# Kernel optimization log

Measured on AMD Instinct MI355X. Metric: run time of the kernel, lower is better.

The kernel has to match this reference:

```python
import jax, jax.numpy as jnp
import numpy as np

BN_EPS = 1e-5


def setup_inputs() -> dict:
    key = jax.random.key(0)
    ks = jax.random.split(key, 6)
    P, D_IN, H, N_NODES = 2_000_000, 3, 128, 20_000
    x = jax.random.normal(ks[0], (P, D_IN), dtype=jnp.float32)
    batch_idx = jax.random.randint(ks[1], (P,), 0, N_NODES, dtype=jnp.int64)
    W1 = jax.random.normal(ks[2], (D_IN, H), dtype=jnp.float32) * 0.5
    b1 = jax.random.normal(ks[3], (H,), dtype=jnp.float32) * 0.1
    gamma = jnp.ones((H,), dtype=jnp.float32)
    beta = jnp.zeros((H,), dtype=jnp.float32)
    running_mean = jnp.zeros((H,), dtype=jnp.float32)
    running_var = jnp.ones((H,), dtype=jnp.float32)
    W2 = jax.random.normal(ks[4], (H, H), dtype=jnp.float32) * (1.0 / np.sqrt(H))
    b2 = jax.random.normal(ks[5], (H,), dtype=jnp.float32) * 0.1
    return {"x": x, "batch_idx": batch_idx, "num_nodes": N_NODES,
            "W1": W1, "b1": b1, "gamma": gamma, "beta": beta,
            "running_mean": running_mean, "running_var": running_var,
            "W2": W2, "b2": b2}


def reference(x, batch_idx, num_nodes, W1, b1, gamma, beta,
              running_mean, running_var, W2, b2):
    # per-point MLP: Linear -> BatchNorm1d (eval: running stats) -> ReLU -> Linear -> ReLU
    h = x @ W1 + b1                                        # [P, H]
    h = (h - running_mean) * jax.lax.rsqrt(running_var + BN_EPS) * gamma + beta
    h = jax.nn.relu(h)
    h = jax.nn.relu(h @ W2 + b2)                            # [P, H], values >= 0
    # scatter_max by node; torch_scatter fills empty segments with 0,
    # and since h >= 0 post-ReLU, clamping the -inf fill to 0 is exact.
    node_feats = jax.ops.segment_max(h, batch_idx, num_segments=num_nodes)
    return jnp.maximum(node_feats, 0.0)                     # [num_nodes, H]
```

## Files before the change

### kernel.cpp

```cpp
#include <hip/hip_runtime.h>
#include <hip/hip_bf16.h>

#define H 128
#define TILE_PTS 32
#define ROW_STRIDE 136
#define NBLK 512
#define BT 1024
#define BSH 4
#define NPB (1 << BSH)
#define CAP 2048
#define RAWN (CAP + 32)
#define HBUF (TILE_PTS * ROW_STRIDE)

typedef __attribute__((ext_vector_type(8))) short short8;
typedef __attribute__((ext_vector_type(4))) float float4v;
typedef __attribute__((ext_vector_type(2))) float float2v;
typedef __attribute__((ext_vector_type(4))) int int4v;
typedef _Float16 half8 __attribute__((ext_vector_type(8)));
typedef _Float16 half2 __attribute__((ext_vector_type(2)));

static __device__ __forceinline__ unsigned short f2bf(float f) {
    unsigned u = __float_as_uint(f);
    unsigned r = (u + 0x7fffu + ((u >> 16) & 1u)) >> 16;
    return (unsigned short)r;
}
static __device__ __forceinline__ unsigned pkbf(float a, float b) {
    __hip_bfloat162 h = __float22bfloat162_rn(float2{a, b});
    return *reinterpret_cast<unsigned*>(&h);
}
static __device__ __forceinline__ unsigned short f2h(float f) {
    _Float16 h = (_Float16)f;
    unsigned short u;
    __builtin_memcpy(&u, &h, 2);
    return u;
}
static __device__ __forceinline__ float h2f(unsigned short us) {
    _Float16 h;
    __builtin_memcpy(&h, &us, 2);
    return (float)h;
}

__global__ __launch_bounds__(BT)
void scatter_slot(const int* __restrict__ bidx, const float* __restrict__ x,
                  const float* __restrict__ W2, unsigned short* __restrict__ W2T,
                  int* __restrict__ gcnt, uint2* __restrict__ xb,
                  int P, int nbuk) {
    extern __shared__ int lh[];
    const int b = blockIdx.x, t = threadIdx.x;
    for (int i = b * BT + t; i < H * H; i += NBLK * BT) {
        int n = i >> 7, k = i & 127;
        W2T[i] = f2h(W2[k * H + n]);
    }
    for (int i = t; i < nbuk; i += BT) lh[i] = 0;
    __syncthreads();
    const int chunk4 = (((P + NBLK - 1) / NBLK) + 3) & ~3;
    const int lo = b * chunk4;
    const int hi = (lo + chunk4 < P) ? lo + chunk4 : P;
    for (int p4 = lo + 4 * t; p4 < hi; p4 += 4 * BT) {
        if (p4 + 4 <= hi) {
            int4v i4 = *(const int4v*)&bidx[p4];
            atomicAdd(&lh[i4.x >> BSH], 1);
            atomicAdd(&lh[i4.y >> BSH], 1);
            atomicAdd(&lh[i4.z >> BSH], 1);
            atomicAdd(&lh[i4.w >> BSH], 1);
        } else {
            for (int p = p4; p < hi; ++p) atomicAdd(&lh[bidx[p] >> BSH], 1);
        }
    }
    __syncthreads();
    for (int i = t; i < nbuk; i += BT) {
        int c = lh[i];
        lh[i] = (c > 0) ? atomicAdd(&gcnt[i], c) : 0;
    }
    __syncthreads();
    auto emit = [&](int idx, float x0, float x1, float x2) {
        int pos = atomicAdd(&lh[idx >> BSH], 1);
        if (pos < CAP) {
            uint2 r;
            r.x = (unsigned)f2h(x0) | ((unsigned)f2h(x1) << 16);
            r.y = (unsigned)f2h(x2) | ((unsigned)(idx & (NPB - 1)) << 16);
            xb[(size_t)(idx >> BSH) * CAP + pos] = r;
        }
    };
    for (int p4 = lo + 4 * t; p4 < hi; p4 += 4 * BT) {
        if (p4 + 4 <= hi) {
            int4v i4 = *(const int4v*)&bidx[p4];
            float4v xa = *(const float4v*)(x + (size_t)p4 * 3);
            float4v xbv = *(const float4v*)(x + (size_t)p4 * 3 + 4);
            float4v xc = *(const float4v*)(x + (size_t)p4 * 3 + 8);
            emit(i4.x, xa[0], xa[1], xa[2]);
            emit(i4.y, xa[3], xbv[0], xbv[1]);
            emit(i4.z, xbv[2], xbv[3], xc[0]);
            emit(i4.w, xc[1], xc[2], xc[3]);
        } else {
            for (int p = p4; p < hi; ++p)
                emit(bidx[p], x[p * 3 + 0], x[p * 3 + 1], x[p * 3 + 2]);
        }
    }
}

__global__ __launch_bounds__(256, 4)
void node_kernel13(const uint2* __restrict__ xb, const int* __restrict__ gcnt,
                   const float* __restrict__ W1, const float* __restrict__ b1,
                   const float* __restrict__ gamma, const float* __restrict__ beta,
                   const float* __restrict__ rmean, const float* __restrict__ rvar,
                   const unsigned short* __restrict__ W2T, const float* __restrict__ b2,
                   float* __restrict__ out, int N)
{
    __shared__ __align__(16) unsigned short pool[2 * HBUF];
    __shared__ __align__(16) uint2 srt[RAWN];
    __shared__ int basec[NPB + 1];
    __shared__ int cur[NPB];

    const int bk   = blockIdx.x;
    const int t    = threadIdx.x;
    const int lane = t & 63;
    const int wave = t >> 6;
    const int g  = t & 15;
    const int q  = t >> 4;
    const int c0 = g * 8;

    half2 w1h[3][4], b1h[4];
    #pragma unroll
    for (int jp = 0; jp < 4; ++jp) {
        #pragma unroll
        for (int e = 0; e < 2; ++e) {
            int c = c0 + 2 * jp + e;
            float sc = gamma[c] * rsqrtf(rvar[c] + 1e-5f);
            w1h[0][jp][e] = (_Float16)(W1[0 * H + c] * sc);
            w1h[1][jp][e] = (_Float16)(W1[1 * H + c] * sc);
            w1h[2][jp][e] = (_Float16)(W1[2 * H + c] * sc);
            b1h[jp][e]    = (_Float16)((b1[c] - rmean[c]) * sc + beta[c]);
        }
    }

    const int bn = lane & 15;
    const int kq = (lane >> 4) * 8;
    half8 bfrag[2][4];
    float  b2v[2];
    #pragma unroll
    for (int nt = 0; nt < 2; ++nt) {
        const int nn = wave * 32 + nt * 16 + bn;
        b2v[nt] = b2[nn];
        #pragma unroll
        for (int kk = 0; kk < 4; ++kk)
            bfrag[nt][kk] = *(const half8*)(const void*)&W2T[nn * H + kk * 32 + kq];
    }

    uint2* raw = (uint2*)pool;
    int n_b = gcnt[bk];
    if (n_b > CAP) n_b = CAP;
    const uint2* src = xb + (size_t)bk * CAP;
    for (int p = t; p < n_b; p += 256) raw[p] = src[p];
    if (t < NPB) cur[t] = 0;
    __syncthreads();
    for (int p = t; p < n_b; p += 256)
        atomicAdd(&cur[raw[p].y >> 16], 1);
    __syncthreads();
    if (t == 0) {
        int run = 0;
        #pragma unroll
        for (int i = 0; i < NPB; ++i) { int c = cur[i]; basec[i] = run; run += c; }
        basec[NPB] = run;
    }
    __syncthreads();
    if (t < NPB) cur[t] = basec[t];
    __syncthreads();
    for (int p = t; p < n_b; p += 256) {
        uint2 r = raw[p];
        int pos = atomicAdd(&cur[r.y >> 16], 1);
        srt[pos] = r;
    }
    for (int p = n_b + t; p < n_b + TILE_PTS; p += 256)
        if (p < RAWN) srt[p] = uint2{0u, 0u};
    __syncthreads();

    const float4v zero4 = {0.f, 0.f, 0.f, 0.f};
    const float NEG_INF = -__builtin_inff();
    const half2 zero2h = {(_Float16)0.f, (_Float16)0.f};
    const int nodebase = bk << BSH;
    const int nlocal = (N - nodebase < NPB) ? (N - nodebase) : NPB;

    const int st0 = q * ROW_STRIDE + c0;
    const int st1 = (q + 16) * ROW_STRIDE + c0;
    const int ar  = bn * ROW_STRIDE + kq;

    #define STAGE_PT(r, hs, so)                                            \
    {                                                                      \
        half2 a0 = __builtin_bit_cast(half2,                               \
            __builtin_amdgcn_perm(0u, (r).x, 0x01000100u));                \
        half2 a1 = __builtin_bit_cast(half2,                               \
            __builtin_amdgcn_perm(0u, (r).x, 0x03020302u));                \
        half2 a2 = __builtin_bit_cast(half2,                               \
            __builtin_amdgcn_perm(0u, (r).y, 0x01000100u));                \
        int4v pk;                                                          \
        _Pragma("unroll")                                                  \
        for (int jp = 0; jp < 4; ++jp) {                                   \
            half2 hh = b1h[jp];                                            \
            hh = __builtin_elementwise_fma(a0, w1h[0][jp], hh);            \
            hh = __builtin_elementwise_fma(a1, w1h[1][jp], hh);            \
            hh = __builtin_elementwise_fma(a2, w1h[2][jp], hh);            \
            hh = __builtin_elementwise_max(hh, zero2h);                    \
            pk[jp] = __builtin_bit_cast(int, hh);                          \
        }                                                                  \
        *(int4v*)(void*)&(hs)[so] = pk;                                    \
    }

    for (int j = 0; j < nlocal; ++j) {
        const int startj = basec[j];
        const int n      = basec[j + 1] - startj;
        const int ntiles = (n + TILE_PTS - 1) >> 5;

        float2v vm0 = {NEG_INF, NEG_INF};
        float2v vm1 = {NEG_INF, NEG_INF};

        if (ntiles > 0) {
            unsigned short* hb = pool;
            unsigned short* hs = pool + HBUF;
            {
                uint2 r0 = srt[startj + q];
                uint2 r1 = srt[startj + q + 16];
                STAGE_PT(r0, hb, st0);
                STAGE_PT(r1, hb, st1);
            }
            __syncthreads();

            for (int tile = 0; tile < ntiles; ++tile) {
                const int tb = tile * TILE_PTS;
                const bool have = (tile + 1 < ntiles);

                uint2 n0, n1;
                if (have) {
                    n0 = srt[startj + tb + TILE_PTS + q];
                    n1 = srt[startj + tb + TILE_PTS + 16 + q];
                }

                float4v acc00, acc01, acc10, acc11;
                {
                    half8 a0v = *(const half8*)(const void*)&hb[ar];
                    half8 a1v = *(const half8*)(const void*)&hb[ar + 16 * ROW_STRIDE];
                    acc00 = __builtin_amdgcn_mfma_f32_16x16x32_f16(a0v, bfrag[0][0], zero4, 0, 0, 0);
                    acc01 = __builtin_amdgcn_mfma_f32_16x16x32_f16(a0v, bfrag[1][0], zero4, 0, 0, 0);
                    acc10 = __builtin_amdgcn_mfma_f32_16x16x32_f16(a1v, bfrag[0][0], zero4, 0, 0, 0);
                    acc11 = __builtin_amdgcn_mfma_f32_16x16x32_f16(a1v, bfrag[1][0], zero4, 0, 0, 0);
                }
                #pragma unroll
                for (int kk = 1; kk < 4; ++kk) {
                    half8 a0v = *(const half8*)(const void*)&hb[ar + kk * 32];
                    half8 a1v = *(const half8*)(const void*)&hb[ar + 16 * ROW_STRIDE + kk * 32];
                    acc00 = __builtin_amdgcn_mfma_f32_16x16x32_f16(a0v, bfrag[0][kk], acc00, 0, 0, 0);
                    acc01 = __builtin_amdgcn_mfma_f32_16x16x32_f16(a0v, bfrag[1][kk], acc01, 0, 0, 0);
                    acc10 = __builtin_amdgcn_mfma_f32_16x16x32_f16(a1v, bfrag[0][kk], acc10, 0, 0, 0);
                    acc11 = __builtin_amdgcn_mfma_f32_16x16x32_f16(a1v, bfrag[1][kk], acc11, 0, 0, 0);
                }

                if (have) {
                    STAGE_PT(n0, hs, st0);
                    STAGE_PT(n1, hs, st1);
                }

                if (tb + TILE_PTS <= n) {
                    vm0 = __builtin_elementwise_max(vm0, float2v{acc00[0], acc00[1]});
                    vm0 = __builtin_elementwise_max(vm0, float2v{acc00[2], acc00[3]});
                    vm0 = __builtin_elementwise_max(vm0, float2v{acc10[0], acc10[1]});
                    vm0 = __builtin_elementwise_max(vm0, float2v{acc10[2], acc10[3]});
                    vm1 = __builtin_elementwise_max(vm1, float2v{acc01[0], acc01[1]});
                    vm1 = __builtin_elementwise_max(vm1, float2v{acc01[2], acc01[3]});
                    vm1 = __builtin_elementwise_max(vm1, float2v{acc11[0], acc11[1]});
                    vm1 = __builtin_elementwise_max(vm1, float2v{acc11[2], acc11[3]});
                } else {
                    const int r0base = (lane >> 4) * 4;
                    #pragma unroll
                    for (int r = 0; r < 4; ++r) {
                        const bool v0 = (tb + r0base + r) < n;
                        const bool v1 = (tb + 16 + r0base + r) < n;
                        vm0[r & 1] = fmaxf(vm0[r & 1], v0 ? acc00[r] : NEG_INF);
                        vm1[r & 1] = fmaxf(vm1[r & 1], v0 ? acc01[r] : NEG_INF);
                        vm0[r & 1] = fmaxf(vm0[r & 1], v1 ? acc10[r] : NEG_INF);
                        vm1[r & 1] = fmaxf(vm1[r & 1], v1 ? acc11[r] : NEG_INF);
                    }
                }
                __syncthreads();
                unsigned short* tmp = hb; hb = hs; hs = tmp;
            }
        }

        float vmax0 = fmaxf(vm0[0], vm0[1]);
        float vmax1 = fmaxf(vm1[0], vm1[1]);
        vmax0 = fmaxf(vmax0, __shfl_xor(vmax0, 16, 64));
        vmax0 = fmaxf(vmax0, __shfl_xor(vmax0, 32, 64));
        vmax1 = fmaxf(vmax1, __shfl_xor(vmax1, 16, 64));
        vmax1 = fmaxf(vmax1, __shfl_xor(vmax1, 32, 64));
        if (lane < 16) {
            float* orow = out + (size_t)(nodebase + j) * H + wave * 32;
            orow[lane]      = fmaxf(vmax0 + b2v[0], 0.f);
            orow[16 + lane] = fmaxf(vmax1 + b2v[1], 0.f);
        }
    }
    #undef STAGE_PT
}

__global__ void histB_kernel(const int* __restrict__ bidx, int* __restrict__ counts, int P) {
    int p = blockIdx.x * 256 + threadIdx.x;
    if (p < P) atomicAdd(&counts[bidx[p]], 1);
}
__global__ __launch_bounds__(1024)
void scanB_kernel(const int* __restrict__ counts, int* __restrict__ starts,
                  int* __restrict__ cursor, int N) {
    __shared__ int sums[1024];
    const int t = threadIdx.x;
    const int chunk = (N + 1023) >> 10;
    const int lo = t * chunk;
    const int hi = (lo + chunk < N) ? lo + chunk : N;
    int s = 0;
    for (int i = lo; i < hi; ++i) s += counts[i];
    sums[t] = s;
    __syncthreads();
    #pragma unroll
    for (int off = 1; off < 1024; off <<= 1) {
        int a = (t >= off) ? sums[t - off] : 0;
        __syncthreads();
        sums[t] += a;
        __syncthreads();
    }
    int run = sums[t] - s;
    for (int i = lo; i < hi; ++i) { starts[i] = run; cursor[i] = run; run += counts[i]; }
    if (t == 1023) starts[N] = sums[1023];
}
__global__ void scatterB_kernel(const int* __restrict__ bidx, const float* __restrict__ x,
                                int* __restrict__ cursor, uint2* __restrict__ xs, int P) {
    int p = blockIdx.x * 256 + threadIdx.x;
    if (p < P) {
        int pos = atomicAdd(&cursor[bidx[p]], 1);
        uint2 r;
        r.x = (unsigned)f2h(x[p * 3 + 0]) | ((unsigned)f2h(x[p * 3 + 1]) << 16);
        r.y = (unsigned)f2h(x[p * 3 + 2]);
        xs[pos] = r;
    }
}
__global__ void convw2_kernel(const float* __restrict__ W2, unsigned short* __restrict__ W2T) {
    int i = blockIdx.x * 256 + threadIdx.x;
    if (i < H * H) {
        int n = i >> 7, k = i & 127;
        W2T[i] = f2bf(W2[k * H + n]);
    }
}

__global__ __launch_bounds__(256, 4)
void node_kernelB(const uint2* __restrict__ xs,
                  const int*   __restrict__ starts,
                  const float* __restrict__ W1, const float* __restrict__ b1,
                  const float* __restrict__ gamma, const float* __restrict__ beta,
                  const float* __restrict__ rmean, const float* __restrict__ rvar,
                  const unsigned short* __restrict__ W2T, const float* __restrict__ b2,
                  float* __restrict__ out, int N)
{
    __shared__ __align__(16) unsigned short h1s[2][TILE_PTS * ROW_STRIDE];
    const int t = threadIdx.x, lane = t & 63, wave = t >> 6;
    const int g = t & 15, q = t >> 4, c0 = g * 8;
    float2v w1f2[3][4], b1f2[4];
    #pragma unroll
    for (int jp = 0; jp < 4; ++jp)
        #pragma unroll
        for (int e = 0; e < 2; ++e) {
            int c = c0 + 2 * jp + e;
            float sc = gamma[c] * rsqrtf(rvar[c] + 1e-5f);
            w1f2[0][jp][e] = W1[0 * H + c] * sc;
            w1f2[1][jp][e] = W1[1 * H + c] * sc;
            w1f2[2][jp][e] = W1[2 * H + c] * sc;
            b1f2[jp][e]    = (b1[c] - rmean[c]) * sc + beta[c];
        }
    const int bn = lane & 15, kq = (lane >> 4) * 8;
    short8 bfrag[2][4]; float b2v[2];
    #pragma unroll
    for (int nt = 0; nt < 2; ++nt) {
        const int nn = wave * 32 + nt * 16 + bn;
        b2v[nt] = b2[nn];
        #pragma unroll
        for (int kk = 0; kk < 4; ++kk)
            bfrag[nt][kk] = *(const short8*)&W2T[nn * H + kk * 32 + kq];
    }
    const float4v zero4 = {0.f, 0.f, 0.f, 0.f};
    const float NEG_INF = -__builtin_inff();
    const float2v zero2 = {0.f, 0.f};
    for (int node = blockIdx.x; node < N; node += gridDim.x) {
        const int start = starts[node];
        const int n = starts[node + 1] - start;
        const int ntiles = (n + TILE_PTS - 1) >> 5;
        float2v vmax2[2];
        vmax2[0] = float2v{NEG_INF, NEG_INF};
        vmax2[1] = float2v{NEG_INF, NEG_INF};
        auto loadx = [&](int tb, float xv[2][3]) {
            #pragma unroll
            for (int i = 0; i < 2; ++i) {
                uint2 r = xs[start + tb + q + 16 * i];
                xv[i][0] = h2f((unsigned short)(r.x & 0xffffu));
                xv[i][1] = h2f((unsigned short)(r.x >> 16));
                xv[i][2] = h2f((unsigned short)(r.y & 0xffffu));
            }
        };
        auto stage = [&](const float xv[2][3], unsigned short* buf) {
            #pragma unroll
            for (int i = 0; i < 2; ++i) {
                const int pl = q + 16 * i;
                float2v a0 = {xv[i][0], xv[i][0]};
                float2v a1 = {xv[i][1], xv[i][1]};
                float2v a2 = {xv[i][2], xv[i][2]};
                int4v pk;
                #pragma unroll
                for (int jp = 0; jp < 4; ++jp) {
                    float2v h = b1f2[jp];
                    h = __builtin_elementwise_fma(a0, w1f2[0][jp], h);
                    h = __builtin_elementwise_fma(a1, w1f2[1][jp], h);
                    h = __builtin_elementwise_fma(a2, w1f2[2][jp], h);
                    h = __builtin_elementwise_max(h, zero2);
                    pk[jp] = (int)pkbf(h[0], h[1]);
                }
                *(int4v*)(void*)&buf[pl * ROW_STRIDE + c0] = pk;
            }
        };
        if (ntiles > 0) {
            float xv[2][3];
            loadx(0, xv);
            stage(xv, h1s[0]);
            __syncthreads();
            int pb = 0;
            for (int tile = 0; tile < ntiles; ++tile) {
                const int tb = tile * TILE_PTS;
                const bool havenext = (tile + 1 < ntiles);
                float nx[2][3];
                if (havenext) loadx(tb + TILE_PTS, nx);
                float4v acc[2][2];
                const unsigned short* hb = h1s[pb];
                {
                    short8 a0 = *(const short8*)&hb[bn * ROW_STRIDE + kq];
                    short8 a1 = *(const short8*)&hb[(16 + bn) * ROW_STRIDE + kq];
                    #pragma unroll
                    for (int nt = 0; nt < 2; ++nt) {
                        acc[0][nt] = __builtin_amdgcn_mfma_f32_16x16x32_bf16(a0, bfrag[nt][0], zero4, 0, 0, 0);
                        acc[1][nt] = __builtin_amdgcn_mfma_f32_16x16x32_bf16(a1, bfrag[nt][0], zero4, 0, 0, 0);
                    }
                }
                #pragma unroll
                for (int kk = 1; kk < 4; ++kk) {
                    short8 a0 = *(const short8*)&hb[bn * ROW_STRIDE + kk * 32 + kq];
                    short8 a1 = *(const short8*)&hb[(16 + bn) * ROW_STRIDE + kk * 32 + kq];
                    #pragma unroll
                    for (int nt = 0; nt < 2; ++nt) {
                        acc[0][nt] = __builtin_amdgcn_mfma_f32_16x16x32_bf16(a0, bfrag[nt][kk], acc[0][nt], 0, 0, 0);
                        acc[1][nt] = __builtin_amdgcn_mfma_f32_16x16x32_bf16(a1, bfrag[nt][kk], acc[1][nt], 0, 0, 0);
                    }
                }
                if (havenext) stage(nx, h1s[pb ^ 1]);
                if (tb + TILE_PTS <= n) {
                    #pragma unroll
                    for (int ps = 0; ps < 2; ++ps)
                        #pragma unroll
                        for (int nt = 0; nt < 2; ++nt) {
                            vmax2[nt] = __builtin_elementwise_max(vmax2[nt],
                                          float2v{acc[ps][nt][0], acc[ps][nt][1]});
                            vmax2[nt] = __builtin_elementwise_max(vmax2[nt],
                                          float2v{acc[ps][nt][2], acc[ps][nt][3]});
                        }
                } else {
                    #pragma unroll
                    for (int ps = 0; ps < 2; ++ps)
                        #pragma unroll
                        for (int r = 0; r < 4; ++r) {
                            const int pl = ps * 16 + (lane >> 4) * 4 + r;
                            const bool valid = (tb + pl) < n;
                            vmax2[0][r & 1] = fmaxf(vmax2[0][r & 1], valid ? acc[ps][0][r] : NEG_INF);
                            vmax2[1][r & 1] = fmaxf(vmax2[1][r & 1], valid ? acc[ps][1][r] : NEG_INF);
                        }
                }
                __syncthreads();
                pb ^= 1;
            }
        }
        float vmax0 = fmaxf(vmax2[0][0], vmax2[0][1]);
        float vmax1 = fmaxf(vmax2[1][0], vmax2[1][1]);
        vmax0 = fmaxf(vmax0, __shfl_xor(vmax0, 16, 64));
        vmax0 = fmaxf(vmax0, __shfl_xor(vmax0, 32, 64));
        vmax1 = fmaxf(vmax1, __shfl_xor(vmax1, 16, 64));
        vmax1 = fmaxf(vmax1, __shfl_xor(vmax1, 32, 64));
        if (lane < 16) {
            float* orow = out + (size_t)node * H + wave * 32;
            orow[lane]      = fmaxf(vmax0 + b2v[0], 0.f);
            orow[16 + lane] = fmaxf(vmax1 + b2v[1], 0.f);
        }
    }
}

extern "C" void kernel_launch(void* const* d_in, const int* in_sizes, int n_in,
                              void* d_out, int out_size, void* d_ws, size_t ws_size,
                              hipStream_t stream) {
    const float* x     = (const float*)d_in[0];
    const int*   bidx  = (const int*)  d_in[1];
    const float* W1    = (const float*)d_in[3];
    const float* b1    = (const float*)d_in[4];
    const float* gamma = (const float*)d_in[5];
    const float* beta  = (const float*)d_in[6];
    const float* rmean = (const float*)d_in[7];
    const float* rvar  = (const float*)d_in[8];
    const float* W2    = (const float*)d_in[9];
    const float* b2    = (const float*)d_in[10];
    float* out = (float*)d_out;

    const int P = in_sizes[1];
    const int N = out_size / H;
    const int nbuk = (N + NPB - 1) >> BSH;

    const size_t szW2T = 32768;
    const size_t szG   = (size_t)4 * ((nbuk + 63) & ~63);
    const size_t szXb  = (size_t)8 * ((size_t)CAP * nbuk + 64);
    const size_t needA = szW2T + szG + szXb + 256;
    const size_t lds1  = (size_t)4 * nbuk;

    char* w = (char*)d_ws;

    if (lds1 <= 60000 && ws_size >= needA) {
        unsigned short* W2T = (unsigned short*)w;
        int* gcnt = (int*)(w + szW2T);
        uint2* xb = (uint2*)(w + szW2T + szG);

        hipMemsetAsync(gcnt, 0, (size_t)nbuk * sizeof(int), stream);
        scatter_slot<<<NBLK, BT, lds1, stream>>>(bidx, x, W2, W2T, gcnt, xb, P, nbuk);
        node_kernel13<<<nbuk, 256, 0, stream>>>(xb, gcnt, W1, b1, gamma, beta,
                                                rmean, rvar, W2T, b2, out, N);
        return;
    }

    const int Npad = (N + 63) & ~63;
    const size_t szStarts = (size_t)4 * (Npad + 64);
    const size_t szCnt    = (size_t)4 * Npad;
    const size_t szRec    = (size_t)8 * (P + 64);
    const size_t needB    = szStarts + szW2T + 2 * szCnt + szRec + 256;
    if (ws_size >= needB) {
        int* starts = (int*)w;
        unsigned short* W2T = (unsigned short*)(w + szStarts);
        int* counts = (int*)(w + szStarts + szW2T);
        int* cursor = (int*)(w + szStarts + szW2T + szCnt);
        uint2* xs   = (uint2*)(w + szStarts + szW2T + 2 * szCnt);

        hipMemsetAsync(counts, 0, (size_t)N * sizeof(int), stream);
        const int pblocks = (P + 255) / 256;
        const int grid = (N < 2048) ? N : 2048;
        convw2_kernel<<<(H * H + 255) / 256, 256, 0, stream>>>(W2, W2T);
        histB_kernel<<<pblocks, 256, 0, stream>>>(bidx, counts, P);
        scanB_kernel<<<1, 1024, 0, stream>>>(counts, starts, cursor, N);
        scatterB_kernel<<<pblocks, 256, 0, stream>>>(bidx, x, cursor, xs, P);
        node_kernelB<<<grid, 256, 0, stream>>>(xs, starts, W1, b1, gamma, beta,
                                               rmean, rvar, W2T, b2, out, N);
    }
}
```

Measured before the change: 217.0 us.

## Switch second-layer GEMM to 32x32x16 MFMA with XOR-swizzled LDS staging

Replaces the four 16x16x32 f16 MFMA accumulators per wave with a single 32x32x16 f16 MFMA chain over eight K-steps. Each lane now owns one output column, so the segment-max reduction needs one shuffle instead of four. The staged hidden rows in LDS are XOR-swizzled to avoid bank conflicts under the new A-fragment read pattern. This trades MFMA shape and register layout for fewer LDS reads and cheaper reductions, at the risk of a longer-latency dependent MFMA chain.

Measured after the change: 223.9 us. 3.1% more time.

```diff
diff --git a/kernel.cpp b/kernel.cpp
--- a/kernel.cpp
+++ b/kernel.cpp
@@ -16,6 +16,7 @@
 typedef __attribute__((ext_vector_type(4))) float float4v;
 typedef __attribute__((ext_vector_type(2))) float float2v;
 typedef __attribute__((ext_vector_type(4))) int int4v;
+typedef __attribute__((ext_vector_type(16))) float f32x16;
 typedef _Float16 half8 __attribute__((ext_vector_type(8)));
 typedef _Float16 half2 __attribute__((ext_vector_type(2)));
 
@@ -100,7 +101,7 @@
 }
 
 __global__ __launch_bounds__(256, 4)
-void node_kernel13(const uint2* __restrict__ xb, const int* __restrict__ gcnt,
+void node_kernel15(const uint2* __restrict__ xb, const int* __restrict__ gcnt,
                    const float* __restrict__ W1, const float* __restrict__ b1,
                    const float* __restrict__ gamma, const float* __restrict__ beta,
                    const float* __restrict__ rmean, const float* __restrict__ rvar,
@@ -134,18 +135,14 @@
         }
     }
 
-    const int bn = lane & 15;
-    const int kq = (lane >> 4) * 8;
-    half8 bfrag[2][4];
-    float  b2v[2];
+    const int col   = lane & 31;
+    const int khalf = lane >> 5;
+    const int nn = wave * 32 + col;
+    half8 bfrag[8];
+    float b2v = b2[nn];
     #pragma unroll
-    for (int nt = 0; nt < 2; ++nt) {
-        const int nn = wave * 32 + nt * 16 + bn;
-        b2v[nt] = b2[nn];
-        #pragma unroll
-        for (int kk = 0; kk < 4; ++kk)
-            bfrag[nt][kk] = *(const half8*)(const void*)&W2T[nn * H + kk * 32 + kq];
-    }
+    for (int kk = 0; kk < 8; ++kk)
+        bfrag[kk] = *(const half8*)(const void*)&W2T[nn * H + kk * 16 + khalf * 8];
 
     uint2* raw = (uint2*)pool;
     int n_b = gcnt[bk];
@@ -175,15 +172,17 @@
         if (p < RAWN) srt[p] = uint2{0u, 0u};
     __syncthreads();
 
-    const float4v zero4 = {0.f, 0.f, 0.f, 0.f};
+    const f32x16 zero16 = {0.f,0.f,0.f,0.f,0.f,0.f,0.f,0.f,
+                           0.f,0.f,0.f,0.f,0.f,0.f,0.f,0.f};
     const float NEG_INF = -__builtin_inff();
     const half2 zero2h = {(_Float16)0.f, (_Float16)0.f};
     const int nodebase = bk << BSH;
     const int nlocal = (N - nodebase < NPB) ? (N - nodebase) : NPB;
 
-    const int st0 = q * ROW_STRIDE + c0;
-    const int st1 = (q + 16) * ROW_STRIDE + c0;
-    const int ar  = bn * ROW_STRIDE + kq;
+    const int swz_st = ((q >> 3) & 1) << 3;
+    const int st0 = q * ROW_STRIDE + (c0 ^ swz_st);
+    const int st1 = (q + 16) * ROW_STRIDE + (c0 ^ swz_st);
+    const int arS = col * ROW_STRIDE + ((khalf ^ ((col >> 3) & 1)) * 8);
 
     #define STAGE_PT(r, hs, so)                                            \
     {                                                                      \
@@ -211,8 +210,7 @@
         const int n      = basec[j + 1] - startj;
         const int ntiles = (n + TILE_PTS - 1) >> 5;
 
-        float2v vm0 = {NEG_INF, NEG_INF};
-        float2v vm1 = {NEG_INF, NEG_INF};
+        float vmx = NEG_INF;
 
         if (ntiles > 0) {
             unsigned short* hb = pool;
@@ -235,23 +233,15 @@
                     n1 = srt[startj + tb + TILE_PTS + 16 + q];
                 }
 
-                float4v acc00, acc01, acc10, acc11;
+                f32x16 acc;
                 {
-                    half8 a0v = *(const half8*)(const void*)&hb[ar];
-                    half8 a1v = *(const half8*)(const void*)&hb[ar + 16 * ROW_STRIDE];
-                    acc00 = __builtin_amdgcn_mfma_f32_16x16x32_f16(a0v, bfrag[0][0], zero4, 0, 0, 0);
-                    acc01 = __builtin_amdgcn_mfma_f32_16x16x32_f16(a0v, bfrag[1][0], zero4, 0, 0, 0);
-                    acc10 = __builtin_amdgcn_mfma_f32_16x16x32_f16(a1v, bfrag[0][0], zero4, 0, 0, 0);
-                    acc11 = __builtin_amdgcn_mfma_f32_16x16x32_f16(a1v, bfrag[1][0], zero4, 0, 0, 0);
+                    half8 a0v = *(const half8*)(const void*)&hb[arS];
+                    acc = __builtin_amdgcn_mfma_f32_32x32x16_f16(a0v, bfrag[0], zero16, 0, 0, 0);
                 }
                 #pragma unroll
-                for (int kk = 1; kk < 4; ++kk) {
-                    half8 a0v = *(const half8*)(const void*)&hb[ar + kk * 32];
-                    half8 a1v = *(const half8*)(const void*)&hb[ar + 16 * ROW_STRIDE + kk * 32];
-                    acc00 = __builtin_amdgcn_mfma_f32_16x16x32_f16(a0v, bfrag[0][kk], acc00, 0, 0, 0);
-                    acc01 = __builtin_amdgcn_mfma_f32_16x16x32_f16(a0v, bfrag[1][kk], acc01, 0, 0, 0);
-                    acc10 = __builtin_amdgcn_mfma_f32_16x16x32_f16(a1v, bfrag[0][kk], acc10, 0, 0, 0);
-                    acc11 = __builtin_amdgcn_mfma_f32_16x16x32_f16(a1v, bfrag[1][kk], acc11, 0, 0, 0);
+                for (int kk = 1; kk < 8; ++kk) {
+                    half8 av = *(const half8*)(const void*)&hb[arS + kk * 16];
+                    acc = __builtin_amdgcn_mfma_f32_32x32x16_f16(av, bfrag[kk], acc, 0, 0, 0);
                 }
 
                 if (have) {
@@ -260,24 +250,14 @@
                 }
 
                 if (tb + TILE_PTS <= n) {
-                    vm0 = __builtin_elementwise_max(vm0, float2v{acc00[0], acc00[1]});
-                    vm0 = __builtin_elementwise_max(vm0, float2v{acc00[2], acc00[3]});
-                    vm0 = __builtin_elementwise_max(vm0, float2v{acc10[0], acc10[1]});
-                    vm0 = __builtin_elementwise_max(vm0, float2v{acc10[2], acc10[3]});
-                    vm1 = __builtin_elementwise_max(vm1, float2v{acc01[0], acc01[1]});
-                    vm1 = __builtin_elementwise_max(vm1, float2v{acc01[2], acc01[3]});
-                    vm1 = __builtin_elementwise_max(vm1, float2v{acc11[0], acc11[1]});
-                    vm1 = __builtin_elementwise_max(vm1, float2v{acc11[2], acc11[3]});
+                    #pragma unroll
+                    for (int i = 0; i < 8; ++i)
+                        vmx = fmaxf(fmaxf(acc[2 * i], acc[2 * i + 1]), vmx);
                 } else {
-                    const int r0base = (lane >> 4) * 4;
                     #pragma unroll
-                    for (int r = 0; r < 4; ++r) {
-                        const bool v0 = (tb + r0base + r) < n;
-                        const bool v1 = (tb + 16 + r0base + r) < n;
-                        vm0[r & 1] = fmaxf(vm0[r & 1], v0 ? acc00[r] : NEG_INF);
-                        vm1[r & 1] = fmaxf(vm1[r & 1], v0 ? acc01[r] : NEG_INF);
-                        vm0[r & 1] = fmaxf(vm0[r & 1], v1 ? acc10[r] : NEG_INF);
-                        vm1[r & 1] = fmaxf(vm1[r & 1], v1 ? acc11[r] : NEG_INF);
+                    for (int r = 0; r < 16; ++r) {
+                        const int row = (r & 3) + 8 * (r >> 2) + 4 * khalf;
+                        vmx = fmaxf(vmx, (tb + row < n) ? acc[r] : NEG_INF);
                     }
                 }
                 __syncthreads();
@@ -285,16 +265,10 @@
             }
         }
 
-        float vmax0 = fmaxf(vm0[0], vm0[1]);
-        float vmax1 = fmaxf(vm1[0], vm1[1]);
-        vmax0 = fmaxf(vmax0, __shfl_xor(vmax0, 16, 64));
-        vmax0 = fmaxf(vmax0, __shfl_xor(vmax0, 32, 64));
-        vmax1 = fmaxf(vmax1, __shfl_xor(vmax1, 16, 64));
-        vmax1 = fmaxf(vmax1, __shfl_xor(vmax1, 32, 64));
-        if (lane < 16) {
+        vmx = fmaxf(vmx, __shfl_xor(vmx, 32, 64));
+        if (lane < 32) {
             float* orow = out + (size_t)(nodebase + j) * H + wave * 32;
-            orow[lane]      = fmaxf(vmax0 + b2v[0], 0.f);
-            orow[16 + lane] = fmaxf(vmax1 + b2v[1], 0.f);
+            orow[lane] = fmaxf(vmx + b2v, 0.f);
         }
     }
     #undef STAGE_PT
@@ -525,7 +499,7 @@
 
         hipMemsetAsync(gcnt, 0, (size_t)nbuk * sizeof(int), stream);
         scatter_slot<<<NBLK, BT, lds1, stream>>>(bidx, x, W2, W2T, gcnt, xb, P, nbuk);
-        node_kernel13<<<nbuk, 256, 0, stream>>>(xb, gcnt, W1, b1, gamma, beta,
+        node_kernel15<<<nbuk, 256, 0, stream>>>(xb, gcnt, W1, b1, gamma, beta,
                                                 rmean, rvar, W2T, b2, out, N);
         return;
     }
```
